# Performance work log

Measured on AMD Instinct MI355X. Metric: run time of the kernel, lower is better.

The kernel has to match this reference:

```python
import jax, jax.numpy as jnp
import numpy as np

N, E, F, C, H, L, ED = 100000, 1600000, 128, 16, 2, 2, 4
EPS = 1e-5
NEG_SLOPE = 0.2


def setup_inputs() -> dict:
    key = jax.random.key(0)
    ks = jax.random.split(key, 32)
    s = 0.1
    inp = {
        "x": jax.random.normal(ks[0], (N, F), dtype=jnp.float32),
        "edge_index": jax.random.randint(ks[1], (2, E), 0, N, dtype=jnp.int64),
        "edge_attr": jax.random.uniform(ks[2], (E, ED), dtype=jnp.float32),
        "embed_W": jax.random.normal(ks[3], (F, C)) * s,
        "embed_b": jnp.zeros((C,), jnp.float32),
        "ln0_w": jnp.ones((C,), jnp.float32),
        "ln0_b": jnp.zeros((C,), jnp.float32),
        "Wl": jax.random.normal(ks[4], (L, C, H * C)) * s,
        "bl": jnp.zeros((L, H * C), jnp.float32),
        "Wr": jax.random.normal(ks[5], (L, C, H * C)) * s,
        "br": jnp.zeros((L, H * C), jnp.float32),
        "We": jax.random.normal(ks[6], (L, ED, H * C)) * s,
        "att": jax.random.normal(ks[7], (L, H, C)) * s,
        "gat_b": jnp.zeros((L, H * C), jnp.float32),
        "n1_w": jnp.ones((L, H * C), jnp.float32),
        "n1_b": jnp.zeros((L, H * C), jnp.float32),
        "lin_W": jax.random.normal(ks[8], (L, H * C, C)) * s,
        "lin_b": jnp.zeros((L, C), jnp.float32),
        "n2_w": jnp.ones((L, C), jnp.float32),
        "n2_b": jnp.zeros((L, C), jnp.float32),
    }
    return inp


def _node_ln(v, w, b):
    # torch.nn.LayerNorm over the feature dim (per node)
    mu = v.mean(-1, keepdims=True)
    var = ((v - mu) ** 2).mean(-1, keepdims=True)
    return (v - mu) / jnp.sqrt(var + EPS) * w + b


def _graph_ln(v, w, b):
    # PyG norm.LayerNorm(mode='graph'): normalize over ALL nodes and channels
    mu = v.mean()
    vc = v - mu
    return vc / jnp.sqrt((vc * vc).mean() + EPS) * w + b


def reference(x, edge_index, edge_attr, embed_W, embed_b, ln0_w, ln0_b,
              Wl, bl, Wr, br, We, att, gat_b, n1_w, n1_b,
              lin_W, lin_b, n2_w, n2_b):
    n = x.shape[0]
    heads, c = att.shape[1], att.shape[2]
    layers = Wl.shape[0]

    # node embedding MLP (dropout = identity in eval)
    h = jax.nn.relu(_node_ln(x @ embed_W + embed_b, ln0_w, ln0_b))

    # add self-loops (fill_value=0.0 -> zero edge features, lin_edge has no bias)
    loop = jnp.arange(n)
    src = jnp.concatenate([edge_index[0], loop])
    dst = jnp.concatenate([edge_index[1], loop])

    hs = [h]
    for i in range(layers):
        xl = (h @ Wl[i] + bl[i]).reshape(n, heads, c)   # source transform (x_j)
        xr = (h @ Wr[i] + br[i]).reshape(n, heads, c)   # target transform (x_i)
        ew = (edge_attr @ We[i]).reshape(-1, heads, c)
        ew = jnp.concatenate([ew, jnp.zeros((n, heads, c), ew.dtype)], axis=0)

        msg = xl[src] + xr[dst] + ew                      # [E+N, H, C]
        logits = jnp.einsum('ehc,hc->eh', jax.nn.leaky_relu(msg, NEG_SLOPE), att[i])
        m = jax.ops.segment_max(logits, dst, num_segments=n)
        ex = jnp.exp(logits - m[dst])
        den = jax.ops.segment_sum(ex, dst, num_segments=n)
        alpha = ex / den[dst]                             # segment softmax over dst

        g = jax.ops.segment_sum(alpha[..., None] * xl[src], dst, num_segments=n)
        g = g.reshape(n, heads * c) + gat_b[i]

        g = jax.nn.relu(_graph_ln(g, n1_w[i], n1_b[i]))
        g = g @ lin_W[i] + lin_b[i]
        g = _graph_ln(g, n2_w[i], n2_b[i])
        h = jax.nn.relu(g + h)                            # residual + relu
        hs.append(h)

    # JumpingKnowledge mode='max': elementwise max over layer outputs
    return jnp.max(jnp.stack(hs, axis=0), axis=0)
```

## Files before the change

### kernel.cpp

```cpp
#include <hip/hip_runtime.h>

#define N_NODES 100000
#define N_EDGES 1600000
#define NF 128
#define NC 16
#define NH 2
#define HC 32
#define NL 2
#define NED 4
#define EPS 1e-5f
#define NEG 0.2f
#define NBUCK 196
#define P1_CHUNK 4096
#define P1_BLKS ((N_EDGES + P1_CHUNK - 1) / P1_CHUNK)
#define AGG_BLKS ((N_NODES + 7) / 8)
#define MID_BLKS ((N_NODES + 15) / 16)

__device__ __forceinline__ unsigned short f2bf(float f) {
    unsigned int u = __float_as_uint(f);
    u += 0x7fffu + ((u >> 16) & 1u);
    return (unsigned short)(u >> 16);
}
__device__ __forceinline__ float bf2f(unsigned short u) {
    return __uint_as_float(((unsigned int)u) << 16);
}
__device__ __forceinline__ unsigned int pack_bf2(float a, float b) {
    return (unsigned int)f2bf(a) | ((unsigned int)f2bf(b) << 16);
}
__device__ __forceinline__ float bflo(int u) {
    return __uint_as_float(((unsigned int)u) << 16);
}
__device__ __forceinline__ float bfhi(int u) {
    return __uint_as_float(((unsigned int)u) & 0xffff0000u);
}
__device__ __forceinline__ float bf_gather(const unsigned short* base, unsigned boff) {
    return bf2f(*(const unsigned short*)((const char*)base + boff));
}

__global__ __launch_bounds__(256) void k_embed(
    const float* __restrict__ x, const float* __restrict__ W,
    const float* __restrict__ b, const float* __restrict__ lnw,
    const float* __restrict__ lnb, float* __restrict__ h, float* __restrict__ jk)
{
    __shared__ __align__(16) float WsT[NC][NF + 4];
    __shared__ __align__(16) float xs[16][NF + 4];
    const int t = threadIdx.x;
    for (int i = t; i < NF * NC; i += 256) {
        int f = i >> 4, c = i & 15;
        WsT[c][f] = W[i];
    }
    const int n0 = blockIdx.x * 16;
    const float4* x4 = (const float4*)x;
    for (int i = t; i < 16 * (NF / 4); i += 256) {
        int r = i >> 5, f4 = i & 31;
        int n = n0 + r;
        float4 v = (n < N_NODES) ? x4[(size_t)n * (NF / 4) + f4]
                                 : make_float4(0.f, 0.f, 0.f, 0.f);
        *(float4*)&xs[r][f4 * 4] = v;
    }
    __syncthreads();
    const int r = t >> 4;
    const int c = t & 15;
    const int n = n0 + r;
    float acc = b[c];
#pragma unroll
    for (int f4 = 0; f4 < NF / 4; ++f4) {
        float4 xv = *(const float4*)&xs[r][f4 * 4];
        float4 wv = *(const float4*)&WsT[c][f4 * 4];
        acc += xv.x * wv.x + xv.y * wv.y + xv.z * wv.z + xv.w * wv.w;
    }
    float s = acc;
    for (int m = 8; m >= 1; m >>= 1) s += __shfl_xor(s, m, 16);
    float mu = s * (1.f / 16.f);
    float d = acc - mu;
    float v = d * d;
    for (int m = 8; m >= 1; m >>= 1) v += __shfl_xor(v, m, 16);
    float inv = rsqrtf(v * (1.f / 16.f) + EPS);
    float out = fmaxf(d * inv * lnw[c] + lnb[c], 0.f);
    if (n < N_NODES) {
        h[(size_t)n * NC + c]  = out;
        jk[(size_t)n * NC + c] = out;
    }
}

__global__ __launch_bounds__(256) void k_bhist(
    const int* __restrict__ dst, int* __restrict__ bcnt)
{
    __shared__ int hist[256];
    const int t = threadIdx.x;
    hist[t] = 0;
    __syncthreads();
    const int e0 = blockIdx.x * P1_CHUNK;
    const int cnt = min(P1_CHUNK, N_EDGES - e0);
    for (int i = t; i < cnt; i += 256)
        atomicAdd(&hist[dst[e0 + i] >> 9], 1);
    __syncthreads();
    if (hist[t] > 0) atomicAdd(&bcnt[t], hist[t]);
}

__global__ __launch_bounds__(256) void k_bscan(
    const int* __restrict__ bcnt, int* __restrict__ bbase, int* __restrict__ bcur)
{
    __shared__ int tmp[256];
    const int t = threadIdx.x;
    int v0 = bcnt[t];
    tmp[t] = v0;
    __syncthreads();
    for (int off = 1; off < 256; off <<= 1) {
        int v = (t >= off) ? tmp[t - off] : 0;
        __syncthreads();
        tmp[t] += v;
        __syncthreads();
    }
    int excl = tmp[t] - v0;
    bbase[t] = excl;
    bcur[t]  = excl;
    if (t == 255) bbase[256] = tmp[t];
}

__global__ __launch_bounds__(256) void k_pass1(
    const int* __restrict__ src, const int* __restrict__ dst,
    const float4* __restrict__ ea4, int* __restrict__ bcur,
    int4* __restrict__ tmp_rec)
{
    __shared__ int2 stage[P1_CHUNK];
    __shared__ unsigned char bstage[P1_CHUNK];
    __shared__ int hist[256];
    __shared__ int exc[256];
    __shared__ int gbase[256];
    __shared__ int scanbuf[256];
    const int t = threadIdx.x;
    const int e0 = blockIdx.x * P1_CHUNK;
    const int cnt = min(P1_CHUNK, N_EDGES - e0);
    hist[t] = 0;
    __syncthreads();
    int mys[16], myb[16], myp[16];
    int nv = 0;
#pragma unroll
    for (int k = 0; k < 16; ++k) {
        int i = k * 256 + t;
        if (i < cnt) {
            int e = e0 + i;
            int d = dst[e];
            mys[nv] = src[e];
            myb[nv] = d >> 9;
            myp[nv] = (e << 9) | (d & 511);
            atomicAdd(&hist[d >> 9], 1);
            ++nv;
        }
    }
    __syncthreads();
    int hv = hist[t];
    scanbuf[t] = hv;
    __syncthreads();
    for (int off = 1; off < 256; off <<= 1) {
        int v = (t >= off) ? scanbuf[t - off] : 0;
        __syncthreads();
        scanbuf[t] += v;
        __syncthreads();
    }
    int ex = scanbuf[t] - hv;
    hist[t] = ex;
    exc[t]  = ex;
    __syncthreads();
    for (int k = 0; k < nv; ++k) {
        int pos = atomicAdd(&hist[myb[k]], 1);
        stage[pos]  = make_int2(mys[k], myp[k]);
        bstage[pos] = (unsigned char)myb[k];
    }
    __syncthreads();
    {
        int c = hist[t] - exc[t];
        gbase[t] = (c > 0) ? atomicAdd(&bcur[t], c) : 0;
    }
    __syncthreads();
    for (int i = t; i < cnt; i += 256) {
        int b = bstage[i];
        int2 se = stage[i];
        int e  = (int)(((unsigned int)se.y) >> 9);
        int dl = se.y & 511;
        float4 ea = ea4[e];
        int gpos = gbase[b] + (i - exc[b]);
        tmp_rec[gpos] = make_int4(se.x, dl,
                                  (int)pack_bf2(ea.x, ea.y),
                                  (int)pack_bf2(ea.z, ea.w));
    }
}

__global__ __launch_bounds__(256) void k_pass2(
    const int* __restrict__ bbase, const int4* __restrict__ tmp_rec,
    int* __restrict__ offsets, int4* __restrict__ csr)
{
    __shared__ int hist[512];
    __shared__ int cur[512];
    __shared__ int scanbuf[256];
    const int b = blockIdx.x, t = threadIdx.x;
    const int ebeg = bbase[b], eend = bbase[b + 1];
    hist[t] = 0; hist[t + 256] = 0;
    __syncthreads();
    for (int i = ebeg + t; i < eend; i += 256)
        atomicAdd(&hist[tmp_rec[i].y], 1);
    __syncthreads();
    int a0 = hist[2 * t], a1 = hist[2 * t + 1];
    int pair = a0 + a1;
    scanbuf[t] = pair;
    __syncthreads();
    for (int off = 1; off < 256; off <<= 1) {
        int v = (t >= off) ? scanbuf[t - off] : 0;
        __syncthreads();
        scanbuf[t] += v;
        __syncthreads();
    }
    int ex2 = scanbuf[t] - pair;
    cur[2 * t]     = ex2;
    cur[2 * t + 1] = ex2 + a0;
    __syncthreads();
    const int n0 = b * 512;
#pragma unroll
    for (int k = 0; k < 2; ++k) {
        int i = t + k * 256;
        int n = n0 + i;
        if (n < N_NODES) offsets[n] = ebeg + cur[i];
    }
    if (b == NBUCK - 1 && t == 0) offsets[N_NODES] = N_EDGES;
    __syncthreads();
    for (int i = ebeg + t; i < eend; i += 256) {
        int4 rec = tmp_rec[i];
        int pos = ebeg + atomicAdd(&cur[rec.y], 1);
        csr[pos] = rec;
    }
}

__global__ __launch_bounds__(256) void k_trans(
    const float* __restrict__ h, const float* __restrict__ Wl, const float* __restrict__ bl,
    const float* __restrict__ Wr, const float* __restrict__ br,
    unsigned short* __restrict__ xl, unsigned short* __restrict__ xr)
{
    __shared__ float Wls[NC * HC], Wrs[NC * HC];
    __shared__ float hs[8][NC + 1];
    const int t = threadIdx.x;
    for (int i = t; i < NC * HC; i += 256) { Wls[i] = Wl[i]; Wrs[i] = Wr[i]; }
    const int n0 = blockIdx.x * 8;
    for (int i = t; i < 8 * NC; i += 256) {
        int r = i >> 4, c = i & 15;
        int n = n0 + r;
        hs[r][c] = (n < N_NODES) ? h[(size_t)n * NC + c] : 0.f;
    }
    __syncthreads();
    const int r = t >> 5;
    const int j = t & 31;
    const int n = n0 + r;
    float al = bl[j], ar = br[j];
#pragma unroll
    for (int c = 0; c < NC; ++c) {
        float hv = hs[r][c];
        al += hv * Wls[c * HC + j];
        ar += hv * Wrs[c * HC + j];
    }
    if (n < N_NODES) {
        xl[(size_t)n * HC + j] = f2bf(al);
        xr[(size_t)n * HC + j] = f2bf(ar);
    }
}

__device__ __forceinline__ float head_sum(float p) {
    p += __shfl_xor(p, 1, 16);
    p += __shfl_xor(p, 2, 16);
    p += __shfl_xor(p, 4, 16);
    p += __shfl_xor(p, 8, 16);
    return p;
}

__global__ __launch_bounds__(256) void k_agg(
    const int* __restrict__ offsets, const int4* __restrict__ csr,
    const float* __restrict__ We, const float* __restrict__ att,
    const float* __restrict__ gat_b,
    const unsigned short* __restrict__ xl, const unsigned short* __restrict__ xr,
    float* __restrict__ g, float2* __restrict__ part)
{
    __shared__ float Wes[NED * HC];
    __shared__ float atts[HC], gbs[HC];
    const int t = threadIdx.x;
    if (t < NED * HC) Wes[t] = We[t];
    if (t < HC) { atts[t] = att[t]; gbs[t] = gat_b[t]; }
    __syncthreads();
    const int grp = t >> 5;
    const int j   = t & 31;
    const int d = blockIdx.x * 8 + grp;
    float gv = 0.f;
    if (d < N_NODES) {
        const float aj = atts[j];
        const float w0 = Wes[j], w1 = Wes[HC + j], w2 = Wes[2 * HC + j], w3 = Wes[3 * HC + j];
        const unsigned jb = (unsigned)(j << 1);
        const float xld = bf_gather(xl, ((unsigned)d << 6) + jb);
        const float xrd = bf_gather(xr, ((unsigned)d << 6) + jb);
        float m = xld + xrd;
        m = fmaxf(m, NEG * m);
        float eh = __expf(head_sum(m * aj));
        float acc = eh * xld;
        float den = eh;
        const int base = offsets[d];
        const int deg  = offsets[d + 1] - base;
        int k = 0;
        for (; k + 4 <= deg; k += 4) {
            const int b0 = base + k;
            const int4 r0 = csr[b0],     r1 = csr[b0 + 1];
            const int4 r2 = csr[b0 + 2], r3 = csr[b0 + 3];
            const float x0 = bf_gather(xl, ((unsigned)r0.x << 6) + jb);
            const float x1 = bf_gather(xl, ((unsigned)r1.x << 6) + jb);
            const float x2 = bf_gather(xl, ((unsigned)r2.x << 6) + jb);
            const float x3 = bf_gather(xl, ((unsigned)r3.x << 6) + jb);
            float m0 = x0 + xrd + bflo(r0.z) * w0 + bfhi(r0.z) * w1 + bflo(r0.w) * w2 + bfhi(r0.w) * w3;
            float m1 = x1 + xrd + bflo(r1.z) * w0 + bfhi(r1.z) * w1 + bflo(r1.w) * w2 + bfhi(r1.w) * w3;
            float m2 = x2 + xrd + bflo(r2.z) * w0 + bfhi(r2.z) * w1 + bflo(r2.w) * w2 + bfhi(r2.w) * w3;
            float m3 = x3 + xrd + bflo(r3.z) * w0 + bfhi(r3.z) * w1 + bflo(r3.w) * w2 + bfhi(r3.w) * w3;
            m0 = fmaxf(m0, NEG * m0);
            m1 = fmaxf(m1, NEG * m1);
            m2 = fmaxf(m2, NEG * m2);
            m3 = fmaxf(m3, NEG * m3);
            float p0 = m0 * aj, p1 = m1 * aj, p2 = m2 * aj, p3 = m3 * aj;
            p0 += __shfl_xor(p0, 1, 16); p1 += __shfl_xor(p1, 1, 16);
            p2 += __shfl_xor(p2, 1, 16); p3 += __shfl_xor(p3, 1, 16);
            p0 += __shfl_xor(p0, 2, 16); p1 += __shfl_xor(p1, 2, 16);
            p2 += __shfl_xor(p2, 2, 16); p3 += __shfl_xor(p3, 2, 16);
            p0 += __shfl_xor(p0, 4, 16); p1 += __shfl_xor(p1, 4, 16);
            p2 += __shfl_xor(p2, 4, 16); p3 += __shfl_xor(p3, 4, 16);
            p0 += __shfl_xor(p0, 8, 16); p1 += __shfl_xor(p1, 8, 16);
            p2 += __shfl_xor(p2, 8, 16); p3 += __shfl_xor(p3, 8, 16);
            const float ee0 = __expf(p0), ee1 = __expf(p1);
            const float ee2 = __expf(p2), ee3 = __expf(p3);
            acc += ee0 * x0 + ee1 * x1 + ee2 * x2 + ee3 * x3;
            den += ee0 + ee1 + ee2 + ee3;
        }
        for (; k < deg; ++k) {
            const int4 r = csr[base + k];
            const float xv = bf_gather(xl, ((unsigned)r.x << 6) + jb);
            float mm = xv + xrd + bflo(r.z) * w0 + bfhi(r.z) * w1 + bflo(r.w) * w2 + bfhi(r.w) * w3;
            mm = fmaxf(mm, NEG * mm);
            const float ee = __expf(head_sum(mm * aj));
            acc += ee * xv;
            den += ee;
        }
        gv = acc / den + gbs[j];
        g[(size_t)d * HC + j] = gv;
    }
    float s = gv, ss = gv * gv;
    for (int m = 32; m >= 1; m >>= 1) { s += __shfl_xor(s, m); ss += __shfl_xor(ss, m); }
    __shared__ float sr[4], ssr[4];
    const int w = t >> 6;
    if ((t & 63) == 0) { sr[w] = s; ssr[w] = ss; }
    __syncthreads();
    if (t == 0) part[blockIdx.x] = make_float2(sr[0] + sr[1] + sr[2] + sr[3],
                                               ssr[0] + ssr[1] + ssr[2] + ssr[3]);
}

__global__ __launch_bounds__(256) void k_red(
    const float2* __restrict__ part, int n, double* __restrict__ out)
{
    const int t = threadIdx.x;
    double s = 0.0, ss = 0.0;
    for (int i = t; i < n; i += 256) {
        float2 p = part[i];
        s += (double)p.x; ss += (double)p.y;
    }
    for (int m = 32; m >= 1; m >>= 1) { s += __shfl_xor(s, m); ss += __shfl_xor(ss, m); }
    __shared__ double sr[4], ssr[4];
    const int w = t >> 6;
    if ((t & 63) == 0) { sr[w] = s; ssr[w] = ss; }
    __syncthreads();
    if (t == 0) {
        out[0] = sr[0] + sr[1] + sr[2] + sr[3];
        out[1] = ssr[0] + ssr[1] + ssr[2] + ssr[3];
    }
}

__global__ __launch_bounds__(256) void k_mid(
    const float* __restrict__ g,
    const float* __restrict__ n1w, const float* __restrict__ n1b,
    const float* __restrict__ linW, const float* __restrict__ linb,
    const double* __restrict__ stats1, float* __restrict__ g2,
    float2* __restrict__ part)
{
    __shared__ float Ws[HC * NC];
    __shared__ float rs[16][HC + 1];
    const int t = threadIdx.x;
    for (int i = t; i < HC * NC; i += 256) Ws[i] = linW[i];
    const double cnt = (double)N_NODES * HC;
    const double mud = stats1[0] / cnt;
    const float mu  = (float)mud;
    const float var = (float)(stats1[1] / cnt - mud * mud);
    const float inv = rsqrtf(var + EPS);
    const int n0 = blockIdx.x * 16;
    for (int i = t; i < 16 * HC; i += 256) {
        int r = i >> 5, j = i & 31;
        int n = n0 + r;
        float v = (n < N_NODES) ? g[(size_t)n * HC + j] : mu;
        v = (v - mu) * inv * n1w[j] + n1b[j];
        rs[r][j] = fmaxf(v, 0.f);
    }
    __syncthreads();
    const int r = t >> 4, c = t & 15;
    const int n = n0 + r;
    float acc = linb[c];
#pragma unroll
    for (int j = 0; j < HC; ++j) acc += rs[r][j] * Ws[j * NC + c];
    float val = (n < N_NODES) ? acc : 0.f;
    if (n < N_NODES) g2[(size_t)n * NC + c] = acc;
    float s = val, ss = val * val;
    for (int m = 32; m >= 1; m >>= 1) { s += __shfl_xor(s, m); ss += __shfl_xor(ss, m); }
    __shared__ float sr[4], ssr[4];
    const int w = t >> 6;
    if ((t & 63) == 0) { sr[w] = s; ssr[w] = ss; }
    __syncthreads();
    if (t == 0) part[blockIdx.x] = make_float2(sr[0] + sr[1] + sr[2] + sr[3],
                                               ssr[0] + ssr[1] + ssr[2] + ssr[3]);
}

__global__ __launch_bounds__(256) void k_ftrans(
    const float* __restrict__ g2, const float* __restrict__ n2w,
    const float* __restrict__ n2b, const double* __restrict__ stats2,
    float* __restrict__ h, float* __restrict__ jk,
    const float* __restrict__ Wl, const float* __restrict__ bl,
    const float* __restrict__ Wr, const float* __restrict__ br,
    unsigned short* __restrict__ xl, unsigned short* __restrict__ xr)
{
    __shared__ float Wls[NC * HC], Wrs[NC * HC];
    __shared__ float hs[8][NC + 1];
    const int t = threadIdx.x;
    for (int i = t; i < NC * HC; i += 256) { Wls[i] = Wl[i]; Wrs[i] = Wr[i]; }
    const double cnt = (double)N_NODES * NC;
    const double mud = stats2[0] / cnt;
    const float mu  = (float)mud;
    const float var = (float)(stats2[1] / cnt - mud * mud);
    const float inv = rsqrtf(var + EPS);
    const int n0 = blockIdx.x * 8;
    if (t < 8 * NC) {
        int r = t >> 4, c = t & 15;
        int n = n0 + r;
        if (n < N_NODES) {
            size_t idx = (size_t)n * NC + c;
            float v = (g2[idx] - mu) * inv * n2w[c] + n2b[c];
            float hn = fmaxf(v + h[idx], 0.f);
            h[idx] = hn;
            jk[idx] = fmaxf(jk[idx], hn);
            hs[r][c] = hn;
        } else hs[r][c] = 0.f;
    }
    __syncthreads();
    const int r = t >> 5;
    const int j = t & 31;
    const int n = n0 + r;
    float al = bl[j], ar = br[j];
#pragma unroll
    for (int c = 0; c < NC; ++c) {
        float hv = hs[r][c];
        al += hv * Wls[c * HC + j];
        ar += hv * Wrs[c * HC + j];
    }
    if (n < N_NODES) {
        xl[(size_t)n * HC + j] = f2bf(al);
        xr[(size_t)n * HC + j] = f2bf(ar);
    }
}

__global__ __launch_bounds__(256) void k_final(
    const float* __restrict__ g2, const float* __restrict__ n2w,
    const float* __restrict__ n2b, const double* __restrict__ stats2,
    float* __restrict__ h, float* __restrict__ jk)
{
    const int i = blockIdx.x * 256 + threadIdx.x;
    if (i >= N_NODES * NC) return;
    const double cnt = (double)N_NODES * NC;
    const double mud = stats2[0] / cnt;
    const float mu  = (float)mud;
    const float var = (float)(stats2[1] / cnt - mud * mud);
    const float inv = rsqrtf(var + EPS);
    const int c = i & (NC - 1);
    float v = (g2[i] - mu) * inv * n2w[c] + n2b[c];
    float hn = fmaxf(v + h[i], 0.f);
    h[i] = hn;
    jk[i] = fmaxf(jk[i], hn);
}

extern "C" void kernel_launch(void* const* d_in, const int* in_sizes, int n_in,
                              void* d_out, int out_size, void* d_ws, size_t ws_size,
                              hipStream_t stream)
{
    const float* x     = (const float*)d_in[0];
    const int*   eidx  = (const int*)d_in[1];
    const float* eattr = (const float*)d_in[2];
    const float* embW  = (const float*)d_in[3];
    const float* embB  = (const float*)d_in[4];
    const float* ln0w  = (const float*)d_in[5];
    const float* ln0b  = (const float*)d_in[6];
    const float* Wl    = (const float*)d_in[7];
    const float* bl    = (const float*)d_in[8];
    const float* Wr    = (const float*)d_in[9];
    const float* br    = (const float*)d_in[10];
    const float* We    = (const float*)d_in[11];
    const float* att   = (const float*)d_in[12];
    const float* gatb  = (const float*)d_in[13];
    const float* n1w   = (const float*)d_in[14];
    const float* n1b   = (const float*)d_in[15];
    const float* linW  = (const float*)d_in[16];
    const float* linb  = (const float*)d_in[17];
    const float* n2w   = (const float*)d_in[18];
    const float* n2b   = (const float*)d_in[19];
    float* out = (float*)d_out;

    char* ws = (char*)d_ws;
    double* stats = (double*)ws;
    char* p = ws + 1024;
    int* bcnt = (int*)p; p += 1024;
    int* bbase = (int*)p; p += 4096;
    int* bcur  = (int*)p; p += 1024;
    int* offsets = (int*)p; p += (size_t)(N_NODES + 64) * 4;
    float* g = (float*)p; p += (size_t)N_NODES * HC * 4;
    int4* csr = (int4*)p; p += (size_t)N_EDGES * 16;
    int4* tmp_rec = (int4*)p;
    char* q = p;
    p += (size_t)N_EDGES * 16;
    float* hq = (float*)q; q += (size_t)N_NODES * NC * 4;
    unsigned short* xlq = (unsigned short*)q; q += (size_t)N_NODES * HC * 2;
    unsigned short* xrq = (unsigned short*)q; q += (size_t)N_NODES * HC * 2;
    float* g2q = (float*)q;
    float2* part1 = (float2*)p; p += (size_t)AGG_BLKS * 8;
    float2* part2 = (float2*)p; p += (size_t)MID_BLKS * 8;

    const int* srcp = eidx;
    const int* dstp = eidx + N_EDGES;

    hipMemsetAsync(bcnt, 0, 1024, stream);
    k_bhist<<<P1_BLKS, 256, 0, stream>>>(dstp, bcnt);
    k_bscan<<<1, 256, 0, stream>>>(bcnt, bbase, bcur);
    k_pass1<<<P1_BLKS, 256, 0, stream>>>(srcp, dstp, (const float4*)eattr,
                                         bcur, tmp_rec);
    k_pass2<<<NBUCK, 256, 0, stream>>>(bbase, tmp_rec, offsets, csr);

    k_embed<<<(N_NODES + 15) / 16, 256, 0, stream>>>(x, embW, embB, ln0w, ln0b, hq, out);

    k_trans<<<(N_NODES + 7) / 8, 256, 0, stream>>>(hq, Wl, bl, Wr, br, xlq, xrq);
    k_agg<<<AGG_BLKS, 256, 0, stream>>>(
        offsets, csr, We, att, gatb, xlq, xrq, g, part1);
    k_red<<<1, 256, 0, stream>>>(part1, AGG_BLKS, stats);
    k_mid<<<MID_BLKS, 256, 0, stream>>>(
        g, n1w, n1b, linW, linb, stats, g2q, part2);
    k_red<<<1, 256, 0, stream>>>(part2, MID_BLKS, stats + 2);
    k_ftrans<<<(N_NODES + 7) / 8, 256, 0, stream>>>(
        g2q, n2w, n2b, stats + 2, hq, out,
        Wl + NC * HC, bl + HC, Wr + NC * HC, br + HC, xlq, xrq);
    k_agg<<<AGG_BLKS, 256, 0, stream>>>(
        offsets, csr, We + NED * HC, att + HC, gatb + HC, xlq, xrq, g, part1);
    k_red<<<1, 256, 0, stream>>>(part1, AGG_BLKS, stats);
    k_mid<<<MID_BLKS, 256, 0, stream>>>(
        g, n1w + HC, n1b + HC, linW + HC * NC, linb + NC, stats, g2q, part2);
    k_red<<<1, 256, 0, stream>>>(part2, MID_BLKS, stats + 2);
    k_final<<<(N_NODES * NC + 255) / 256, 256, 0, stream>>>(
        g2q, n2w + NC, n2b + NC, stats + 2, hq, out);
}
```

Baseline: 479.1 us.

## Process two channels per thread in aggregation and fuse stat reductions via tickets

The aggregation kernel now handles 16 nodes per block, with each thread processing two adjacent channels through 32-bit bf16-pair gathers and packed float2 math. This halves the gather instructions and cuts the head-sum shuffles from four steps to three. The separate single-block reduction kernels are removed: the last block of k_agg and k_mid, chosen by an atomic ticket, sums the per-block partials, which drops four kernel launches. The cost is extra atomics and fences, plus ticket counters that must be zeroed each call.

```diff
diff --git a/kernel.cpp b/kernel.cpp
--- a/kernel.cpp
+++ b/kernel.cpp
@@ -13,8 +13,10 @@
 #define NBUCK 196
 #define P1_CHUNK 4096
 #define P1_BLKS ((N_EDGES + P1_CHUNK - 1) / P1_CHUNK)
-#define AGG_BLKS ((N_NODES + 7) / 8)
+#define AGG_BLKS ((N_NODES + 15) / 16)
 #define MID_BLKS ((N_NODES + 15) / 16)
+
+typedef __attribute__((ext_vector_type(2))) float f32x2;
 
 __device__ __forceinline__ unsigned short f2bf(float f) {
     unsigned int u = __float_as_uint(f);
@@ -33,8 +35,13 @@
 __device__ __forceinline__ float bfhi(int u) {
     return __uint_as_float(((unsigned int)u) & 0xffff0000u);
 }
-__device__ __forceinline__ float bf_gather(const unsigned short* base, unsigned boff) {
-    return bf2f(*(const unsigned short*)((const char*)base + boff));
+__device__ __forceinline__ f32x2 sp2(float v) { f32x2 r; r.x = v; r.y = v; return r; }
+__device__ __forceinline__ f32x2 bf2_gather(const unsigned short* base, unsigned boff) {
+    unsigned u = *(const unsigned*)((const char*)base + boff);
+    f32x2 r;
+    r.x = __uint_as_float(u << 16);
+    r.y = __uint_as_float(u & 0xffff0000u);
+    return r;
 }
 
 __global__ __launch_bounds__(256) void k_embed(
@@ -263,11 +270,10 @@
     }
 }
 
-__device__ __forceinline__ float head_sum(float p) {
-    p += __shfl_xor(p, 1, 16);
-    p += __shfl_xor(p, 2, 16);
-    p += __shfl_xor(p, 4, 16);
-    p += __shfl_xor(p, 8, 16);
+__device__ __forceinline__ float hsum8(float p) {
+    p += __shfl_xor(p, 1, 8);
+    p += __shfl_xor(p, 2, 8);
+    p += __shfl_xor(p, 4, 8);
     return p;
 }
 
@@ -276,7 +282,8 @@
     const float* __restrict__ We, const float* __restrict__ att,
     const float* __restrict__ gat_b,
     const unsigned short* __restrict__ xl, const unsigned short* __restrict__ xr,
-    float* __restrict__ g, float2* __restrict__ part)
+    float* __restrict__ g, float2* __restrict__ part,
+    unsigned* __restrict__ done, double* __restrict__ outstats)
 {
     __shared__ float Wes[NED * HC];
     __shared__ float atts[HC], gbs[HC];
@@ -284,20 +291,24 @@
     if (t < NED * HC) Wes[t] = We[t];
     if (t < HC) { atts[t] = att[t]; gbs[t] = gat_b[t]; }
     __syncthreads();
-    const int grp = t >> 5;
-    const int j   = t & 31;
-    const int d = blockIdx.x * 8 + grp;
-    float gv = 0.f;
+    const int grp = t >> 4;
+    const int j2  = t & 15;
+    const int d = blockIdx.x * 16 + grp;
+    f32x2 gv = sp2(0.f);
     if (d < N_NODES) {
-        const float aj = atts[j];
-        const float w0 = Wes[j], w1 = Wes[HC + j], w2 = Wes[2 * HC + j], w3 = Wes[3 * HC + j];
-        const unsigned jb = (unsigned)(j << 1);
-        const float xld = bf_gather(xl, ((unsigned)d << 6) + jb);
-        const float xrd = bf_gather(xr, ((unsigned)d << 6) + jb);
-        float m = xld + xrd;
-        m = fmaxf(m, NEG * m);
-        float eh = __expf(head_sum(m * aj));
-        float acc = eh * xld;
+        f32x2 aj; aj.x = atts[2 * j2]; aj.y = atts[2 * j2 + 1];
+        f32x2 w0; w0.x = Wes[2 * j2];          w0.y = Wes[2 * j2 + 1];
+        f32x2 w1; w1.x = Wes[HC + 2 * j2];     w1.y = Wes[HC + 2 * j2 + 1];
+        f32x2 w2; w2.x = Wes[2 * HC + 2 * j2]; w2.y = Wes[2 * HC + 2 * j2 + 1];
+        f32x2 w3; w3.x = Wes[3 * HC + 2 * j2]; w3.y = Wes[3 * HC + 2 * j2 + 1];
+        const unsigned jb = (unsigned)(j2 << 2);
+        const f32x2 xld = bf2_gather(xl, ((unsigned)d << 6) + jb);
+        const f32x2 xrd = bf2_gather(xr, ((unsigned)d << 6) + jb);
+        f32x2 m = xld + xrd;
+        m.x = fmaxf(m.x, NEG * m.x);
+        m.y = fmaxf(m.y, NEG * m.y);
+        float eh = __expf(hsum8(m.x * aj.x + m.y * aj.y));
+        f32x2 acc = sp2(eh) * xld;
         float den = eh;
         const int base = offsets[d];
         const int deg  = offsets[d + 1] - base;
@@ -306,71 +317,85 @@
             const int b0 = base + k;
             const int4 r0 = csr[b0],     r1 = csr[b0 + 1];
             const int4 r2 = csr[b0 + 2], r3 = csr[b0 + 3];
-            const float x0 = bf_gather(xl, ((unsigned)r0.x << 6) + jb);
-            const float x1 = bf_gather(xl, ((unsigned)r1.x << 6) + jb);
-            const float x2 = bf_gather(xl, ((unsigned)r2.x << 6) + jb);
-            const float x3 = bf_gather(xl, ((unsigned)r3.x << 6) + jb);
-            float m0 = x0 + xrd + bflo(r0.z) * w0 + bfhi(r0.z) * w1 + bflo(r0.w) * w2 + bfhi(r0.w) * w3;
-            float m1 = x1 + xrd + bflo(r1.z) * w0 + bfhi(r1.z) * w1 + bflo(r1.w) * w2 + bfhi(r1.w) * w3;
-            float m2 = x2 + xrd + bflo(r2.z) * w0 + bfhi(r2.z) * w1 + bflo(r2.w) * w2 + bfhi(r2.w) * w3;
-            float m3 = x3 + xrd + bflo(r3.z) * w0 + bfhi(r3.z) * w1 + bflo(r3.w) * w2 + bfhi(r3.w) * w3;
-            m0 = fmaxf(m0, NEG * m0);
-            m1 = fmaxf(m1, NEG * m1);
-            m2 = fmaxf(m2, NEG * m2);
-            m3 = fmaxf(m3, NEG * m3);
-            float p0 = m0 * aj, p1 = m1 * aj, p2 = m2 * aj, p3 = m3 * aj;
-            p0 += __shfl_xor(p0, 1, 16); p1 += __shfl_xor(p1, 1, 16);
-            p2 += __shfl_xor(p2, 1, 16); p3 += __shfl_xor(p3, 1, 16);
-            p0 += __shfl_xor(p0, 2, 16); p1 += __shfl_xor(p1, 2, 16);
-            p2 += __shfl_xor(p2, 2, 16); p3 += __shfl_xor(p3, 2, 16);
-            p0 += __shfl_xor(p0, 4, 16); p1 += __shfl_xor(p1, 4, 16);
-            p2 += __shfl_xor(p2, 4, 16); p3 += __shfl_xor(p3, 4, 16);
-            p0 += __shfl_xor(p0, 8, 16); p1 += __shfl_xor(p1, 8, 16);
-            p2 += __shfl_xor(p2, 8, 16); p3 += __shfl_xor(p3, 8, 16);
+            const f32x2 x0 = bf2_gather(xl, ((unsigned)r0.x << 6) + jb);
+            const f32x2 x1 = bf2_gather(xl, ((unsigned)r1.x << 6) + jb);
+            const f32x2 x2 = bf2_gather(xl, ((unsigned)r2.x << 6) + jb);
+            const f32x2 x3 = bf2_gather(xl, ((unsigned)r3.x << 6) + jb);
+            f32x2 m0 = x0 + xrd, m1 = x1 + xrd, m2 = x2 + xrd, m3 = x3 + xrd;
+            m0 += sp2(bflo(r0.z)) * w0; m1 += sp2(bflo(r1.z)) * w0;
+            m2 += sp2(bflo(r2.z)) * w0; m3 += sp2(bflo(r3.z)) * w0;
+            m0 += sp2(bfhi(r0.z)) * w1; m1 += sp2(bfhi(r1.z)) * w1;
+            m2 += sp2(bfhi(r2.z)) * w1; m3 += sp2(bfhi(r3.z)) * w1;
+            m0 += sp2(bflo(r0.w)) * w2; m1 += sp2(bflo(r1.w)) * w2;
+            m2 += sp2(bflo(r2.w)) * w2; m3 += sp2(bflo(r3.w)) * w2;
+            m0 += sp2(bfhi(r0.w)) * w3; m1 += sp2(bfhi(r1.w)) * w3;
+            m2 += sp2(bfhi(r2.w)) * w3; m3 += sp2(bfhi(r3.w)) * w3;
+            m0.x = fmaxf(m0.x, NEG * m0.x); m0.y = fmaxf(m0.y, NEG * m0.y);
+            m1.x = fmaxf(m1.x, NEG * m1.x); m1.y = fmaxf(m1.y, NEG * m1.y);
+            m2.x = fmaxf(m2.x, NEG * m2.x); m2.y = fmaxf(m2.y, NEG * m2.y);
+            m3.x = fmaxf(m3.x, NEG * m3.x); m3.y = fmaxf(m3.y, NEG * m3.y);
+            float p0 = m0.x * aj.x + m0.y * aj.y;
+            float p1 = m1.x * aj.x + m1.y * aj.y;
+            float p2 = m2.x * aj.x + m2.y * aj.y;
+            float p3 = m3.x * aj.x + m3.y * aj.y;
+            p0 += __shfl_xor(p0, 1, 8); p1 += __shfl_xor(p1, 1, 8);
+            p2 += __shfl_xor(p2, 1, 8); p3 += __shfl_xor(p3, 1, 8);
+            p0 += __shfl_xor(p0, 2, 8); p1 += __shfl_xor(p1, 2, 8);
+            p2 += __shfl_xor(p2, 2, 8); p3 += __shfl_xor(p3, 2, 8);
+            p0 += __shfl_xor(p0, 4, 8); p1 += __shfl_xor(p1, 4, 8);
+            p2 += __shfl_xor(p2, 4, 8); p3 += __shfl_xor(p3, 4, 8);
             const float ee0 = __expf(p0), ee1 = __expf(p1);
             const float ee2 = __expf(p2), ee3 = __expf(p3);
-            acc += ee0 * x0 + ee1 * x1 + ee2 * x2 + ee3 * x3;
+            acc += sp2(ee0) * x0; acc += sp2(ee1) * x1;
+            acc += sp2(ee2) * x2; acc += sp2(ee3) * x3;
             den += ee0 + ee1 + ee2 + ee3;
         }
         for (; k < deg; ++k) {
             const int4 r = csr[base + k];
-            const float xv = bf_gather(xl, ((unsigned)r.x << 6) + jb);
-            float mm = xv + xrd + bflo(r.z) * w0 + bfhi(r.z) * w1 + bflo(r.w) * w2 + bfhi(r.w) * w3;
-            mm = fmaxf(mm, NEG * mm);
-            const float ee = __expf(head_sum(mm * aj));
-            acc += ee * xv;
+            const f32x2 xv = bf2_gather(xl, ((unsigned)r.x << 6) + jb);
+            f32x2 mm = xv + xrd;
+            mm += sp2(bflo(r.z)) * w0; mm += sp2(bfhi(r.z)) * w1;
+            mm += sp2(bflo(r.w)) * w2; mm += sp2(bfhi(r.w)) * w3;
+            mm.x = fmaxf(mm.x, NEG * mm.x); mm.y = fmaxf(mm.y, NEG * mm.y);
+            const float ee = __expf(hsum8(mm.x * aj.x + mm.y * aj.y));
+            acc += sp2(ee) * xv;
             den += ee;
         }
-        gv = acc / den + gbs[j];
-        g[(size_t)d * HC + j] = gv;
-    }
-    float s = gv, ss = gv * gv;
+        const float invd = 1.f / den;
+        gv.x = acc.x * invd + gbs[2 * j2];
+        gv.y = acc.y * invd + gbs[2 * j2 + 1];
+        *(float2*)&g[(size_t)d * HC + 2 * j2] = make_float2(gv.x, gv.y);
+    }
+    float s = gv.x + gv.y, ss = gv.x * gv.x + gv.y * gv.y;
     for (int m = 32; m >= 1; m >>= 1) { s += __shfl_xor(s, m); ss += __shfl_xor(ss, m); }
     __shared__ float sr[4], ssr[4];
+    __shared__ unsigned lastblk;
     const int w = t >> 6;
     if ((t & 63) == 0) { sr[w] = s; ssr[w] = ss; }
     __syncthreads();
-    if (t == 0) part[blockIdx.x] = make_float2(sr[0] + sr[1] + sr[2] + sr[3],
-                                               ssr[0] + ssr[1] + ssr[2] + ssr[3]);
-}
-
-__global__ __launch_bounds__(256) void k_red(
-    const float2* __restrict__ part, int n, double* __restrict__ out)
-{
-    const int t = threadIdx.x;
-    double s = 0.0, ss = 0.0;
-    for (int i = t; i < n; i += 256) {
-        float2 p = part[i];
-        s += (double)p.x; ss += (double)p.y;
-    }
-    for (int m = 32; m >= 1; m >>= 1) { s += __shfl_xor(s, m); ss += __shfl_xor(ss, m); }
-    __shared__ double sr[4], ssr[4];
-    const int w = t >> 6;
-    if ((t & 63) == 0) { sr[w] = s; ssr[w] = ss; }
-    __syncthreads();
     if (t == 0) {
-        out[0] = sr[0] + sr[1] + sr[2] + sr[3];
-        out[1] = ssr[0] + ssr[1] + ssr[2] + ssr[3];
+        part[blockIdx.x] = make_float2(sr[0] + sr[1] + sr[2] + sr[3],
+                                       ssr[0] + ssr[1] + ssr[2] + ssr[3]);
+        __threadfence();
+        lastblk = (atomicAdd(done, 1u) == (unsigned)gridDim.x - 1u) ? 1u : 0u;
+    }
+    __syncthreads();
+    if (lastblk) {
+        __threadfence();
+        double rs = 0.0, rss = 0.0;
+        const int nb = (int)gridDim.x;
+        for (int i = t; i < nb; i += 256) {
+            float2 pp = part[i];
+            rs += (double)pp.x; rss += (double)pp.y;
+        }
+        for (int m = 32; m >= 1; m >>= 1) { rs += __shfl_xor(rs, m); rss += __shfl_xor(rss, m); }
+        __shared__ double dsr[4], dssr[4];
+        if ((t & 63) == 0) { dsr[w] = rs; dssr[w] = rss; }
+        __syncthreads();
+        if (t == 0) {
+            outstats[0] = dsr[0] + dsr[1] + dsr[2] + dsr[3];
+            outstats[1] = dssr[0] + dssr[1] + dssr[2] + dssr[3];
+        }
     }
 }
 
@@ -379,10 +404,11 @@
     const float* __restrict__ n1w, const float* __restrict__ n1b,
     const float* __restrict__ linW, const float* __restrict__ linb,
     const double* __restrict__ stats1, float* __restrict__ g2,
-    float2* __restrict__ part)
+    float2* __restrict__ part, unsigned* __restrict__ done,
+    double* __restrict__ outstats)
 {
     __shared__ float Ws[HC * NC];
-    __shared__ float rs[16][HC + 1];
+    __shared__ float rs_[16][HC + 1];
     const int t = threadIdx.x;
     for (int i = t; i < HC * NC; i += 256) Ws[i] = linW[i];
     const double cnt = (double)N_NODES * HC;
@@ -396,24 +422,47 @@
         int n = n0 + r;
         float v = (n < N_NODES) ? g[(size_t)n * HC + j] : mu;
         v = (v - mu) * inv * n1w[j] + n1b[j];
-        rs[r][j] = fmaxf(v, 0.f);
+        rs_[r][j] = fmaxf(v, 0.f);
     }
     __syncthreads();
     const int r = t >> 4, c = t & 15;
     const int n = n0 + r;
     float acc = linb[c];
 #pragma unroll
-    for (int j = 0; j < HC; ++j) acc += rs[r][j] * Ws[j * NC + c];
+    for (int j = 0; j < HC; ++j) acc += rs_[r][j] * Ws[j * NC + c];
     float val = (n < N_NODES) ? acc : 0.f;
     if (n < N_NODES) g2[(size_t)n * NC + c] = acc;
     float s = val, ss = val * val;
     for (int m = 32; m >= 1; m >>= 1) { s += __shfl_xor(s, m); ss += __shfl_xor(ss, m); }
     __shared__ float sr[4], ssr[4];
+    __shared__ unsigned lastblk;
     const int w = t >> 6;
     if ((t & 63) == 0) { sr[w] = s; ssr[w] = ss; }
     __syncthreads();
-    if (t == 0) part[blockIdx.x] = make_float2(sr[0] + sr[1] + sr[2] + sr[3],
-                                               ssr[0] + ssr[1] + ssr[2] + ssr[3]);
+    if (t == 0) {
+        part[blockIdx.x] = make_float2(sr[0] + sr[1] + sr[2] + sr[3],
+                                       ssr[0] + ssr[1] + ssr[2] + ssr[3]);
+        __threadfence();
+        lastblk = (atomicAdd(done, 1u) == (unsigned)gridDim.x - 1u) ? 1u : 0u;
+    }
+    __syncthreads();
+    if (lastblk) {
+        __threadfence();
+        double rs = 0.0, rss = 0.0;
+        const int nb = (int)gridDim.x;
+        for (int i = t; i < nb; i += 256) {
+            float2 pp = part[i];
+            rs += (double)pp.x; rss += (double)pp.y;
+        }
+        for (int m = 32; m >= 1; m >>= 1) { rs += __shfl_xor(rs, m); rss += __shfl_xor(rss, m); }
+        __shared__ double dsr[4], dssr[4];
+        if ((t & 63) == 0) { dsr[w] = rs; dssr[w] = rss; }
+        __syncthreads();
+        if (t == 0) {
+            outstats[0] = dsr[0] + dsr[1] + dsr[2] + dsr[3];
+            outstats[1] = dssr[0] + dssr[1] + dssr[2] + dssr[3];
+        }
+    }
 }
 
 __global__ __launch_bounds__(256) void k_ftrans(
@@ -510,6 +559,7 @@
 
     char* ws = (char*)d_ws;
     double* stats = (double*)ws;
+    unsigned* tickets = (unsigned*)(ws + 64);
     char* p = ws + 1024;
     int* bcnt = (int*)p; p += 1024;
     int* bbase = (int*)p; p += 4096;
@@ -531,6 +581,7 @@
     const int* dstp = eidx + N_EDGES;
 
     hipMemsetAsync(bcnt, 0, 1024, stream);
+    hipMemsetAsync(tickets, 0, 16, stream);
     k_bhist<<<P1_BLKS, 256, 0, stream>>>(dstp, bcnt);
     k_bscan<<<1, 256, 0, stream>>>(bcnt, bbase, bcur);
     k_pass1<<<P1_BLKS, 256, 0, stream>>>(srcp, dstp, (const float4*)eattr,
@@ -541,20 +592,18 @@
 
     k_trans<<<(N_NODES + 7) / 8, 256, 0, stream>>>(hq, Wl, bl, Wr, br, xlq, xrq);
     k_agg<<<AGG_BLKS, 256, 0, stream>>>(
-        offsets, csr, We, att, gatb, xlq, xrq, g, part1);
-    k_red<<<1, 256, 0, stream>>>(part1, AGG_BLKS, stats);
+        offsets, csr, We, att, gatb, xlq, xrq, g, part1, tickets + 0, stats);
     k_mid<<<MID_BLKS, 256, 0, stream>>>(
-        g, n1w, n1b, linW, linb, stats, g2q, part2);
-    k_red<<<1, 256, 0, stream>>>(part2, MID_BLKS, stats + 2);
+        g, n1w, n1b, linW, linb, stats, g2q, part2, tickets + 1, stats + 2);
     k_ftrans<<<(N_NODES + 7) / 8, 256, 0, stream>>>(
         g2q, n2w, n2b, stats + 2, hq, out,
         Wl + NC * HC, bl + HC, Wr + NC * HC, br + HC, xlq, xrq);
     k_agg<<<AGG_BLKS, 256, 0, stream>>>(
-        offsets, csr, We + NED * HC, att + HC, gatb + HC, xlq, xrq, g, part1);
-    k_red<<<1, 256, 0, stream>>>(part1, AGG_BLKS, stats);
+        offsets, csr, We + NED * HC, att + HC, gatb + HC, xlq, xrq, g, part1,
+        tickets + 2, stats);
     k_mid<<<MID_BLKS, 256, 0, stream>>>(
-        g, n1w + HC, n1b + HC, linW + HC * NC, linb + NC, stats, g2q, part2);
-    k_red<<<1, 256, 0, stream>>>(part2, MID_BLKS, stats + 2);
+        g, n1w + HC, n1b + HC, linW + HC * NC, linb + NC, stats, g2q, part2,
+        tickets + 3, stats + 2);
     k_final<<<(N_NODES * NC + 255) / 256, 256, 0, stream>>>(
         g2q, n2w + NC, n2b + NC, stats + 2, hq, out);
 }
```

Measured after the change: 1.038 ms. 2.17x slower.
